# Optimization experiments

Measured on AMD Instinct MI355X. Metric: run time of the kernel, lower is better.

The kernel has to match this reference:

```python
import jax, jax.numpy as jnp
import numpy as np

N_NODES = 10000
N_EDGES = 160000
F = 128
NRB = 32


def setup_inputs() -> dict:
    key = jax.random.key(0)
    ks = jax.random.split(key, 20)
    inp = {
        "s": jax.random.normal(ks[0], (N_NODES, F), jnp.float32),
        "v": jax.random.normal(ks[1], (N_NODES, 3, F), jnp.float32),
        "radial_embeddings_1": jax.random.normal(ks[2], (N_EDGES, NRB), jnp.float32),
        "radial_embeddings_2": jax.random.normal(ks[3], (N_EDGES, NRB), jnp.float32),
        "radial_embeddings_3": jax.random.normal(ks[4], (N_EDGES, NRB), jnp.float32),
        "f_cut_1": jax.random.uniform(ks[5], (N_EDGES,), jnp.float32),
        "f_cut_2": jax.random.uniform(ks[6], (N_EDGES,), jnp.float32),
        "f_cut_3": jax.random.uniform(ks[7], (N_EDGES,), jnp.float32),
        "unit_vectors_1": jax.random.normal(ks[8], (N_EDGES, 3), jnp.float32),
        "unit_vectors_2": jax.random.normal(ks[9], (N_EDGES, 3), jnp.float32),
        "unit_vectors_3": jax.random.normal(ks[10], (N_EDGES, 3), jnp.float32),
        "edge_index": jax.random.randint(ks[11], (2, N_EDGES), 0, N_NODES, jnp.int64),
    }
    # parameters (Linear uses y = x @ W.T + b; we store transposed for x @ W)
    sc1 = 1.0 / np.sqrt(F)
    sc2 = 1.0 / np.sqrt(NRB)
    inp["W1"] = jax.random.uniform(ks[12], (F, F), jnp.float32, -sc1, sc1)
    inp["b1"] = jax.random.uniform(ks[13], (F,), jnp.float32, -sc1, sc1)
    inp["W2"] = jax.random.uniform(ks[14], (F, 8 * F), jnp.float32, -sc1, sc1)
    inp["b2"] = jax.random.uniform(ks[15], (8 * F,), jnp.float32, -sc1, sc1)
    inp["Wr"] = jax.random.uniform(ks[16], (NRB, 8 * F), jnp.float32, -sc2, sc2)
    inp["br"] = jax.random.uniform(ks[17], (8 * F,), jnp.float32, -sc2, sc2)
    return inp


def reference(s, v, radial_embeddings_1, radial_embeddings_2, radial_embeddings_3,
              f_cut_1, f_cut_2, f_cut_3,
              unit_vectors_1, unit_vectors_2, unit_vectors_3,
              edge_index, W1, b1, W2, b2, Wr, br):
    idx_i, idx_j = edge_index[0], edge_index[1]
    n_nodes = s.shape[0]
    nf = W1.shape[0]

    # phi = Linear(F,F) -> SiLU -> Linear(F,8F)   [N, 8F]
    phi = jax.nn.silu(s @ W1 + b1) @ W2 + b2

    # shared-weight radial filter over 3 branches  [E, 8F]
    W = ((radial_embeddings_1 @ Wr + br) * f_cut_1[:, None]
         + (radial_embeddings_2 @ Wr + br) * f_cut_2[:, None]
         + (radial_embeddings_3 @ Wr + br) * f_cut_3[:, None])

    x = phi[idx_j] * W                                    # [E, 8F]
    x_s, x_vv, x_vs1, x_vs2, x_vs3, x_vc1, x_vc2, x_vc3 = jnp.split(x, 8, axis=-1)

    ds = jax.ops.segment_sum(x_s, idx_i, num_segments=n_nodes)

    vj = v[idx_j]                                         # [E, 3, F]
    ex = lambda a: a[:, None, :]                          # [E,1,F] broadcast over xyz
    cr = lambda u: jnp.cross(vj, u[..., None], axis=1)    # [E, 3, F]

    x_v = (vj * ex(x_vv)
           + ex(x_vs1) * unit_vectors_1[..., None]
           + ex(x_vs2) * unit_vectors_2[..., None]
           + ex(x_vs3) * unit_vectors_3[..., None]
           + ex(x_vc1) * cr(unit_vectors_1)
           + ex(x_vc2) * cr(unit_vectors_2)
           + ex(x_vc3) * cr(unit_vectors_3))              # [E, 3, F]

    dv = jax.ops.segment_sum(x_v, idx_i, num_segments=n_nodes)
    return (s + ds, v + dv)
```

## Files before the change

### kernel.cpp

```cpp
#include <hip/hip_runtime.h>

#define N_NODES 10000
#define N_EDGES 160000
#define MAXT     19400
#define NSLOT    (MAXT * 16 + 16)
#define MSG_GRID 5000
#define PHI_BLOCKS 628
#define RC_BLOCKS 5000
#define PAD_BLOCKS 625

typedef __attribute__((ext_vector_type(8))) __bf16 bf16x8;
typedef __attribute__((ext_vector_type(8))) unsigned short u16x8;
typedef __attribute__((ext_vector_type(4))) float f32x4;

static __device__ __forceinline__ unsigned short f2bf(float x) {
    union { float f; unsigned u; } un;
    un.f = x;
    unsigned r = un.u + 0x7fffu + ((un.u >> 16) & 1u);
    return (unsigned short)(r >> 16);
}

static __device__ __forceinline__ float bf2f(unsigned short h) {
    union { unsigned u; float f; } un;
    un.u = ((unsigned)h) << 16;
    return un.f;
}

__global__ __launch_bounds__(256) void init_kernel(
    const float* __restrict__ s, const float* __restrict__ v,
    const int* __restrict__ eix,
    const float* __restrict__ W1, const float* __restrict__ W2,
    const float* __restrict__ Wr,
    float* __restrict__ out0, float* __restrict__ out1,
    unsigned short* __restrict__ vbf2, int* __restrict__ cnt,
    unsigned short* __restrict__ W1T, unsigned short* __restrict__ W2T,
    unsigned short* __restrict__ WrT)
{
    int tid = blockIdx.x * 256 + threadIdx.x;
    if (tid < N_NODES * 96)
        reinterpret_cast<float4*>(out1)[tid] = reinterpret_cast<const float4*>(v)[tid];
    if (tid < N_NODES * 32)
        reinterpret_cast<float4*>(out0)[tid] = reinterpret_cast<const float4*>(s)[tid];
    if (tid < N_NODES * 128) {
        int n = tid >> 7, f = tid & 127;
        ushort4 q;
        q.x = f2bf(v[(size_t)n * 384 + f]);
        q.y = f2bf(v[(size_t)n * 384 + 128 + f]);
        q.z = f2bf(v[(size_t)n * 384 + 256 + f]);
        q.w = 0;
        *reinterpret_cast<ushort4*>(vbf2 + (size_t)tid * 4) = q;
    }
    if (tid < 131072) {
        int n = tid >> 7, k = tid & 127;
        W2T[tid] = f2bf(W2[k * 1024 + n]);
    }
    if (tid < 16384) {
        int n = tid >> 7, k = tid & 127;
        W1T[tid] = f2bf(W1[k * 128 + n]);
    }
    if (tid < 32768) {
        int n = tid >> 5, k = tid & 31;
        WrT[tid] = f2bf(Wr[k * 1024 + n]);
    }
    if (tid < N_EDGES) atomicAdd(&cnt[eix[tid]], 1);
}

__global__ __launch_bounds__(1024) void scan_kernel(
    const int* __restrict__ cnt, int* __restrict__ cursor,
    int* __restrict__ nb, int* __restrict__ tile_node,
    int* __restrict__ ntiles)
{
    __shared__ int ws[16];
    __shared__ int run_s;
    int t = threadIdx.x, lane = t & 63, wid = t >> 6;
    if (t == 0) run_s = 0;
    __syncthreads();
    for (int base = 0; base < N_NODES; base += 1024) {
        int idx = base + t;
        int deg = (idx < N_NODES) ? cnt[idx] : 0;
        int tc = (deg + 15) >> 4;
        int x = tc;
        #pragma unroll
        for (int o = 1; o < 64; o <<= 1) {
            int y = __shfl_up(x, o);
            if (lane >= o) x += y;
        }
        if (lane == 63) ws[wid] = x;
        __syncthreads();
        if (wid == 0) {
            int wv = (lane < 16) ? ws[lane] : 0;
            #pragma unroll
            for (int o = 1; o < 16; o <<= 1) {
                int y = __shfl_up(wv, o);
                if (lane >= o) wv += y;
            }
            if (lane < 16) ws[lane] = wv;
        }
        __syncthreads();
        int wb = wid ? ws[wid - 1] : 0;
        int ex = run_s + wb + x - tc;
        if (idx < N_NODES) {
            nb[idx] = ex * 16;
            cursor[idx] = ex * 16;
            for (int k = 0; k < tc; ++k) tile_node[ex + k] = idx;
        }
        __syncthreads();
        if (t == 0) run_s += ws[15];
        __syncthreads();
    }
    if (t == 0) *ntiles = run_s;
}

__global__ __launch_bounds__(256) void rc_phi_kernel(
    const float* __restrict__ R1, const float* __restrict__ R2,
    const float* __restrict__ R3,
    const float* __restrict__ f1, const float* __restrict__ f2,
    const float* __restrict__ f3,
    const float* __restrict__ u1, const float* __restrict__ u2,
    const float* __restrict__ u3,
    const int* __restrict__ eix, const int* __restrict__ cnt,
    const int* __restrict__ nb, int* __restrict__ cursor,
    unsigned short* __restrict__ Rc_s, float* __restrict__ hdr,
    const float* __restrict__ s, const unsigned short* __restrict__ W1T,
    const float* __restrict__ b1, const unsigned short* __restrict__ W2T,
    const float* __restrict__ b2, unsigned short* __restrict__ phi2)
{
    __shared__ unsigned short h_lds[64][136];
    int bx = blockIdx.x;

    if (bx < PHI_BLOCKS) {
        int t = threadIdx.x, lane = t & 63, w = t >> 6;
        int quad = lane >> 4, l16 = lane & 15;
        int m0 = (bx >> 2) * 64;
        int colg = bx & 3;

        int arow = m0 + w * 16 + l16;
        if (arow > N_NODES - 1) arow = N_NODES - 1;
        bf16x8 afr[4];
        #pragma unroll
        for (int ks = 0; ks < 4; ++ks) {
            const float* sp = s + (size_t)arow * 128 + ks * 32 + quad * 8;
            #pragma unroll
            for (int jj = 0; jj < 8; ++jj) afr[ks][jj] = (__bf16)sp[jj];
        }
        #pragma unroll
        for (int cg = 0; cg < 8; ++cg) {
            int col = cg * 16 + l16;
            f32x4 acc = {0.f, 0.f, 0.f, 0.f};
            #pragma unroll
            for (int ks = 0; ks < 4; ++ks) {
                bf16x8 bf = *reinterpret_cast<const bf16x8*>(W1T + (size_t)col * 128 + ks * 32 + quad * 8);
                acc = __builtin_amdgcn_mfma_f32_16x16x32_bf16(afr[ks], bf, acc, 0, 0, 0);
            }
            float bb = b1[col];
            #pragma unroll
            for (int r = 0; r < 4; ++r) {
                int row = w * 16 + quad * 4 + r;
                float val = acc[r] + bb;
                h_lds[row][col] = f2bf(val / (1.f + __expf(-val)));
            }
        }
        __syncthreads();

        bf16x8 a2[4][4];
        #pragma unroll
        for (int rg = 0; rg < 4; ++rg)
            #pragma unroll
            for (int ks = 0; ks < 4; ++ks)
                a2[rg][ks] = *reinterpret_cast<const bf16x8*>(&h_lds[rg * 16 + l16][ks * 32 + quad * 8]);
        #pragma unroll
        for (int i = 0; i < 4; ++i) {
            int col = colg * 256 + w * 64 + i * 16 + l16;
            f32x4 acc2[4] = {{0,0,0,0},{0,0,0,0},{0,0,0,0},{0,0,0,0}};
            #pragma unroll
            for (int ks = 0; ks < 4; ++ks) {
                bf16x8 bf = *reinterpret_cast<const bf16x8*>(W2T + (size_t)col * 128 + ks * 32 + quad * 8);
                #pragma unroll
                for (int rg = 0; rg < 4; ++rg)
                    acc2[rg] = __builtin_amdgcn_mfma_f32_16x16x32_bf16(a2[rg][ks], bf, acc2[rg], 0, 0, 0);
            }
            float bb = b2[col];
            int f = col & 127, cc = col >> 7;
            #pragma unroll
            for (int rg = 0; rg < 4; ++rg)
                #pragma unroll
                for (int r = 0; r < 4; ++r) {
                    int row = m0 + rg * 16 + quad * 4 + r;
                    if (row < N_NODES)
                        phi2[(size_t)row * 1024 + f * 8 + cc] = f2bf(acc2[rg][r] + bb);
                }
        }
        return;
    }

    bx -= PHI_BLOCKS;
    if (bx >= RC_BLOCKS) {
        int t2 = (bx - RC_BLOCKS) * 256 + threadIdx.x;
        int n = t2 >> 4, r = t2 & 15;
        int deg = cnt[n], tc = (deg + 15) >> 4;
        int p = deg + r;
        if (p < tc * 16) {
            size_t slot = (size_t)nb[n] + p;
            f32x4 z = {0.f, 0.f, 0.f, 0.f};
            f32x4* hp = reinterpret_cast<f32x4*>(hdr + slot * 16);
            hp[0] = z; hp[1] = z; hp[2] = z; hp[3] = z;
            f32x4* rp = reinterpret_cast<f32x4*>(Rc_s + slot * 32);
            rp[0] = z; rp[1] = z; rp[2] = z; rp[3] = z;
        }
        return;
    }

    int tid = bx * 256 + threadIdx.x;
    int e = tid >> 3, sub = tid & 7;
    int lane = threadIdx.x & 63;
    float a = f1[e], b = f2[e], c = f3[e];
    int k0 = sub * 4;
    float4 r1 = *reinterpret_cast<const float4*>(R1 + (size_t)e * 32 + k0);
    float4 r2 = *reinterpret_cast<const float4*>(R2 + (size_t)e * 32 + k0);
    float4 r3 = *reinterpret_cast<const float4*>(R3 + (size_t)e * 32 + k0);
    ushort4 o;
    o.x = f2bf(r1.x * a + r2.x * b + r3.x * c);
    o.y = f2bf(r1.y * a + r2.y * b + r3.y * c);
    o.z = f2bf(r1.z * a + r2.z * b + r3.z * c);
    o.w = f2bf(r1.w * a + r2.w * b + r3.w * c);
    int slot = 0;
    if (sub == 0) slot = atomicAdd(&cursor[eix[e]], 1);
    slot = __shfl(slot, lane & 56);
    *reinterpret_cast<ushort4*>(Rc_s + (size_t)slot * 32 + k0) = o;
    if (sub == 0) {
        float4 h;
        h.x = __int_as_float(eix[N_EDGES + e]);
        h.y = a + b + c;
        h.z = 0.f; h.w = 0.f;
        *reinterpret_cast<float4*>(hdr + (size_t)slot * 16) = h;
    } else if (sub < 4) {
        const float* up = (sub == 1 ? u1 : (sub == 2 ? u2 : u3)) + (size_t)e * 3;
        float4 h;
        h.x = up[0]; h.y = up[1]; h.z = up[2]; h.w = 0.f;
        *reinterpret_cast<float4*>(hdr + (size_t)slot * 16 + (size_t)sub * 4) = h;
    }
}

__global__ __launch_bounds__(512) void msg_kernel(
    const unsigned short* __restrict__ Rc_s, const float* __restrict__ hdr,
    const unsigned short* __restrict__ phi2, const unsigned short* __restrict__ vbf2,
    const unsigned short* __restrict__ WrT, const float* __restrict__ br,
    const int* __restrict__ tile_node, const int* __restrict__ ntiles,
    float* __restrict__ out0, float* __restrict__ out1)
{
    int t = threadIdx.x, lane = t & 63, w = t >> 6;
    int quad = lane >> 4, l16 = lane & 15;
    int fcol = w * 16 + l16;
    const int nt = *ntiles;

    bf16x8 bfrag[8];
    float brv[8];
    #pragma unroll
    for (int c = 0; c < 8; ++c) {
        int col = c * 128 + fcol;
        bfrag[c] = *reinterpret_cast<const bf16x8*>(WrT + (size_t)col * 32 + quad * 8);
        brv[c] = br[col];
    }

    __shared__ float srow[2][16][16];

    for (int t4 = 0; t4 < 4; ++t4) {
        int tile = blockIdx.x + t4 * MSG_GRID;
        if (tile >= nt) break;
        int node = tile_node[tile];
        size_t s0 = (size_t)tile * 16;
        int p = t4 & 1;

        if (t < 256) srow[p][t >> 4][t & 15] = hdr[s0 * 16 + t];

        bf16x8 af = *reinterpret_cast<const bf16x8*>(Rc_s + (s0 + l16) * 32 + quad * 8);
        f32x4 acc[8];
        #pragma unroll
        for (int c = 0; c < 8; ++c) {
            f32x4 z = {0.f, 0.f, 0.f, 0.f};
            acc[c] = __builtin_amdgcn_mfma_f32_16x16x32_bf16(af, bfrag[c], z, 0, 0, 0);
        }

        __syncthreads();

        float ds = 0.f, d0 = 0.f, d1 = 0.f, d2 = 0.f;
        #pragma unroll
        for (int r = 0; r < 4; ++r) {
            int row = quad * 4 + r;
            int j = __float_as_int(srow[p][row][0]);
            float fs = srow[p][row][1];
            size_t o = (size_t)j * 128 + fcol;
            u16x8 ph = *reinterpret_cast<const u16x8*>(phi2 + o * 8);
            ushort4 vb = *reinterpret_cast<const ushort4*>(vbf2 + o * 4);
            float x[8];
            #pragma unroll
            for (int c = 0; c < 8; ++c)
                x[c] = bf2f(ph[c]) * (acc[c][r] + brv[c] * fs);
            float vjx = bf2f(vb.x), vjy = bf2f(vb.y), vjz = bf2f(vb.z);
            float u1x = srow[p][row][4],  u1y = srow[p][row][5],  u1z = srow[p][row][6];
            float u2x = srow[p][row][8],  u2y = srow[p][row][9],  u2z = srow[p][row][10];
            float u3x = srow[p][row][12], u3y = srow[p][row][13], u3z = srow[p][row][14];
            float qx = x[5] * u1x + x[6] * u2x + x[7] * u3x;
            float qy = x[5] * u1y + x[6] * u2y + x[7] * u3y;
            float qz = x[5] * u1z + x[6] * u2z + x[7] * u3z;
            ds += x[0];
            d0 += x[1] * vjx + x[2] * u1x + x[3] * u2x + x[4] * u3x + vjy * qz - vjz * qy;
            d1 += x[1] * vjy + x[2] * u1y + x[3] * u2y + x[4] * u3y + vjz * qx - vjx * qz;
            d2 += x[1] * vjz + x[2] * u1z + x[3] * u2z + x[4] * u3z + vjx * qy - vjy * qx;
        }

        ds += __shfl_xor(ds, 16); ds += __shfl_xor(ds, 32);
        d0 += __shfl_xor(d0, 16); d0 += __shfl_xor(d0, 32);
        d1 += __shfl_xor(d1, 16); d1 += __shfl_xor(d1, 32);
        d2 += __shfl_xor(d2, 16); d2 += __shfl_xor(d2, 32);

        if (quad == 0) {
            atomicAdd(&out0[(size_t)node * 128 + fcol], ds);
            size_t vo = (size_t)node * 384 + fcol;
            atomicAdd(&out1[vo], d0);
            atomicAdd(&out1[vo + 128], d1);
            atomicAdd(&out1[vo + 256], d2);
        }
    }
}

extern "C" void kernel_launch(void* const* d_in, const int* in_sizes, int n_in,
                              void* d_out, int out_size, void* d_ws, size_t ws_size,
                              hipStream_t stream) {
    const float* s  = (const float*)d_in[0];
    const float* v  = (const float*)d_in[1];
    const float* R1 = (const float*)d_in[2];
    const float* R2 = (const float*)d_in[3];
    const float* R3 = (const float*)d_in[4];
    const float* f1 = (const float*)d_in[5];
    const float* f2 = (const float*)d_in[6];
    const float* f3 = (const float*)d_in[7];
    const float* u1 = (const float*)d_in[8];
    const float* u2 = (const float*)d_in[9];
    const float* u3 = (const float*)d_in[10];
    const int*  eix = (const int*)d_in[11];
    const float* W1 = (const float*)d_in[12];
    const float* b1 = (const float*)d_in[13];
    const float* W2 = (const float*)d_in[14];
    const float* b2 = (const float*)d_in[15];
    const float* Wr = (const float*)d_in[16];
    const float* br = (const float*)d_in[17];

    char* ws = (char*)d_ws;
    size_t off = 0;
    auto alloc = [&](size_t bytes) -> void* {
        void* p = ws + off;
        off = (off + bytes + 255) & ~(size_t)255;
        return p;
    };
    int* cnt       = (int*)alloc((size_t)N_NODES * 4);
    int* cursor    = (int*)alloc((size_t)N_NODES * 4);
    int* nb        = (int*)alloc((size_t)N_NODES * 4);
    int* tile_node = (int*)alloc((size_t)MAXT * 4);
    int* ntiles    = (int*)alloc(4);
    unsigned short* Rc_s = (unsigned short*)alloc((size_t)NSLOT * 32 * 2);
    float* hdr           = (float*)alloc((size_t)NSLOT * 16 * 4);
    unsigned short* vbf2 = (unsigned short*)alloc((size_t)N_NODES * 128 * 4 * 2);
    unsigned short* phi2 = (unsigned short*)alloc((size_t)N_NODES * 1024 * 2);
    unsigned short* W1T  = (unsigned short*)alloc(128 * 128 * 2);
    unsigned short* W2T  = (unsigned short*)alloc(1024 * 128 * 2);
    unsigned short* WrT  = (unsigned short*)alloc(1024 * 32 * 2);
    (void)ws_size; (void)in_sizes; (void)n_in; (void)out_size;

    float* out0 = (float*)d_out;
    float* out1 = out0 + (size_t)N_NODES * 128;

    hipMemsetAsync(cnt, 0, (size_t)N_NODES * 4, stream);
    init_kernel<<<5000, 256, 0, stream>>>(s, v, eix, W1, W2, Wr,
                                          out0, out1, vbf2, cnt, W1T, W2T, WrT);
    scan_kernel<<<1, 1024, 0, stream>>>(cnt, cursor, nb, tile_node, ntiles);
    rc_phi_kernel<<<PHI_BLOCKS + RC_BLOCKS + PAD_BLOCKS, 256, 0, stream>>>(
        R1, R2, R3, f1, f2, f3, u1, u2, u3, eix, cnt, nb, cursor, Rc_s, hdr,
        s, W1T, b1, W2T, b2, phi2);
    msg_kernel<<<MSG_GRID, 512, 0, stream>>>(Rc_s, hdr, phi2, vbf2, WrT, br,
                                             tile_node, ntiles, out0, out1);
}
```

Baseline: 360.3 us.

## Software-pipeline tile header and Rc fragment loads in message kernel

Restructures the message kernel's tile loop so the header row and the A-fragment for the next tile are prefetched into the alternate shared buffer while the current tile is being computed. The loop becomes unbounded with a single sync per iteration, and the padded shared row width avoids bank conflicts. The cross product is also reordered algebraically into per-unit-vector terms, and the tile_node load moves to the atomic section. This adds register pressure and changes the floating-point summation order.

```diff
diff --git a/kernel.cpp b/kernel.cpp
--- a/kernel.cpp
+++ b/kernel.cpp
@@ -262,18 +262,19 @@
         brv[c] = br[col];
     }
 
-    __shared__ float srow[2][16][16];
-
-    for (int t4 = 0; t4 < 4; ++t4) {
-        int tile = blockIdx.x + t4 * MSG_GRID;
-        if (tile >= nt) break;
-        int node = tile_node[tile];
-        size_t s0 = (size_t)tile * 16;
-        int p = t4 & 1;
-
-        if (t < 256) srow[p][t >> 4][t & 15] = hdr[s0 * 16 + t];
-
-        bf16x8 af = *reinterpret_cast<const bf16x8*>(Rc_s + (s0 + l16) * 32 + quad * 8);
+    __shared__ float srow[2][16][17];
+
+    int tile = blockIdx.x;
+    bf16x8 af;
+    if (tile < nt) {
+        if (t < 256) srow[0][t >> 4][t & 15] = hdr[(size_t)tile * 256 + t];
+        af = *reinterpret_cast<const bf16x8*>(Rc_s + ((size_t)tile * 16 + l16) * 32 + quad * 8);
+    }
+
+    for (int k = 0; tile < nt; ++k, tile += MSG_GRID) {
+        int p = k & 1;
+        __syncthreads();
+
         f32x4 acc[8];
         #pragma unroll
         for (int c = 0; c < 8; ++c) {
@@ -281,7 +282,11 @@
             acc[c] = __builtin_amdgcn_mfma_f32_16x16x32_bf16(af, bfrag[c], z, 0, 0, 0);
         }
 
-        __syncthreads();
+        int tn = tile + MSG_GRID;
+        if (tn < nt) {
+            if (t < 256) srow[p ^ 1][t >> 4][t & 15] = hdr[(size_t)tn * 256 + t];
+            af = *reinterpret_cast<const bf16x8*>(Rc_s + ((size_t)tn * 16 + l16) * 32 + quad * 8);
+        }
 
         float ds = 0.f, d0 = 0.f, d1 = 0.f, d2 = 0.f;
         #pragma unroll
@@ -300,13 +305,20 @@
             float u1x = srow[p][row][4],  u1y = srow[p][row][5],  u1z = srow[p][row][6];
             float u2x = srow[p][row][8],  u2y = srow[p][row][9],  u2z = srow[p][row][10];
             float u3x = srow[p][row][12], u3y = srow[p][row][13], u3z = srow[p][row][14];
-            float qx = x[5] * u1x + x[6] * u2x + x[7] * u3x;
-            float qy = x[5] * u1y + x[6] * u2y + x[7] * u3y;
-            float qz = x[5] * u1z + x[6] * u2z + x[7] * u3z;
+
             ds += x[0];
-            d0 += x[1] * vjx + x[2] * u1x + x[3] * u2x + x[4] * u3x + vjy * qz - vjz * qy;
-            d1 += x[1] * vjy + x[2] * u1y + x[3] * u2y + x[4] * u3y + vjz * qx - vjx * qz;
-            d2 += x[1] * vjz + x[2] * u1z + x[3] * u2z + x[4] * u3z + vjx * qy - vjy * qx;
+            d0 += vjx * x[1] + u1x * x[2] + u2x * x[3] + u3x * x[4]
+                + x[5] * (vjy * u1z - vjz * u1y)
+                + x[6] * (vjy * u2z - vjz * u2y)
+                + x[7] * (vjy * u3z - vjz * u3y);
+            d1 += vjy * x[1] + u1y * x[2] + u2y * x[3] + u3y * x[4]
+                + x[5] * (vjz * u1x - vjx * u1z)
+                + x[6] * (vjz * u2x - vjx * u2z)
+                + x[7] * (vjz * u3x - vjx * u3z);
+            d2 += vjz * x[1] + u1z * x[2] + u2z * x[3] + u3z * x[4]
+                + x[5] * (vjx * u1y - vjy * u1x)
+                + x[6] * (vjx * u2y - vjy * u2x)
+                + x[7] * (vjx * u3y - vjy * u3x);
         }
 
         ds += __shfl_xor(ds, 16); ds += __shfl_xor(ds, 32);
@@ -315,6 +327,7 @@
         d2 += __shfl_xor(d2, 16); d2 += __shfl_xor(d2, 32);
 
         if (quad == 0) {
+            int node = tile_node[tile];
             atomicAdd(&out0[(size_t)node * 128 + fcol], ds);
             size_t vo = (size_t)node * 384 + fcol;
             atomicAdd(&out1[vo], d0);
```

Result: faster. 321.8 us (-10.7%).
